# Kernel optimization log

Measured on AMD Instinct MI355X. Metric: run time of the kernel, lower is better.

## Reference

```python
import jax, jax.numpy as jnp
import numpy as np

B, S, D_VAL, D_AT = 4, 4096, 256, 256


def setup_inputs() -> dict:
    key = jax.random.key(0)
    k1, k2, k3, k4 = jax.random.split(key, 4)
    x = jax.random.normal(k1, (B, S, D_VAL), dtype=jnp.float32)
    # nn.Linear(d_in, d_out, bias=False) weight has shape [d_out, d_in]; y = x @ W.T
    Wq = jax.random.normal(k2, (D_AT, D_VAL), dtype=jnp.float32) * (1.0 / np.sqrt(D_VAL))
    Wk = jax.random.normal(k3, (D_AT, D_VAL), dtype=jnp.float32) * (1.0 / np.sqrt(D_VAL))
    Wv = jax.random.normal(k4, (D_VAL, D_VAL), dtype=jnp.float32) * (1.0 / np.sqrt(D_VAL))
    return {"x": x, "Wq": Wq, "Wk": Wk, "Wv": Wv}


def reference(x, Wq, Wk, Wv):
    # projections (Linear, no bias): x @ W.T
    q = jnp.einsum('bsd,ad->bsa', x, Wq)   # [B,S,d_at]
    k = jnp.einsum('bsd,ad->bsa', x, Wk)   # [B,S,d_at]
    v = jnp.einsum('bsd,ed->bse', x, Wv)   # [B,S,d_val]
    scale = 1.0 / jnp.sqrt(jnp.asarray(q.shape[-1], dtype=q.dtype))
    scores = jnp.einsum('bqa,bka->bqk', q, k) * scale  # [B,S,S]
    weights = jax.nn.softmax(scores, axis=-1)
    out = jnp.einsum('bqk,bke->bqe', weights, v)       # [B,S,d_val]
    return out
```

## Files before the change

kernel.cpp:

```cpp
#include <hip/hip_runtime.h>
#include <stdint.h>

#define B_ 4
#define S_ 4096
#define D_ 256
#define M_ (B_*S_)

typedef __attribute__((ext_vector_type(8))) short bf16x8;
typedef __attribute__((ext_vector_type(8))) unsigned short u16x8;
typedef __attribute__((ext_vector_type(4))) float f32x4;
typedef __attribute__((ext_vector_type(4))) unsigned short u16x4;

static __device__ __forceinline__ unsigned short f2bf(float f) {
  union { float f; unsigned u; } v; v.f = f;
  unsigned r = v.u + 0x7fffu + ((v.u >> 16) & 1u);
  return (unsigned short)(r >> 16);
}
static __device__ __forceinline__ float bf2f(unsigned short h) {
  union { unsigned u; float f; } v; v.u = ((unsigned)h) << 16;
  return v.f;
}

__global__ void cvt_kernel(const float* __restrict__ src, unsigned short* __restrict__ dst,
                           int n4) {
  int i = blockIdx.x * blockDim.x + threadIdx.x;
  int stride = gridDim.x * blockDim.x;
  for (; i < n4; i += stride) {
    float4 v = reinterpret_cast<const float4*>(src)[i];
    u16x4 o;
    o.x = f2bf(v.x); o.y = f2bf(v.y);
    o.z = f2bf(v.z); o.w = f2bf(v.w);
    reinterpret_cast<u16x4*>(dst)[i] = o;
  }
}

__global__ void cvt_w_kernel(const float* __restrict__ Wq, const float* __restrict__ Wk,
                             const float* __restrict__ Wv,
                             unsigned short* __restrict__ wqb, unsigned short* __restrict__ wkb,
                             unsigned short* __restrict__ wvb) {
  const int m = blockIdx.y;
  const float* src = (m == 0) ? Wq : (m == 1) ? Wk : Wv;
  unsigned short* dst = (m == 0) ? wqb : (m == 1) ? wkb : wvb;
  const float scale = (m == 0) ? 0.0625f * 1.44269504f : 1.0f;
  int i = blockIdx.x * 256 + threadIdx.x;
  int frag = i >> 6, lane = i & 63;
  int kc = frag >> 4, n = frag & 15;
  int lr = lane & 15, lh = lane >> 4;
  const float* sp = src + (size_t)(n * 16 + lr) * D_ + kc * 32 + lh * 8;
  float4 a = reinterpret_cast<const float4*>(sp)[0];
  float4 b = reinterpret_cast<const float4*>(sp)[1];
  u16x8 o;
  o[0] = f2bf(a.x * scale); o[1] = f2bf(a.y * scale);
  o[2] = f2bf(a.z * scale); o[3] = f2bf(a.w * scale);
  o[4] = f2bf(b.x * scale); o[5] = f2bf(b.y * scale);
  o[6] = f2bf(b.z * scale); o[7] = f2bf(b.w * scale);
  *reinterpret_cast<u16x8*>(dst + (size_t)frag * 512 + lane * 8) = o;
}

__global__ __launch_bounds__(256, 3) void proj_kernel(
    const unsigned short* __restrict__ xb,
    const unsigned short* __restrict__ wq,
    const unsigned short* __restrict__ wk,
    const unsigned short* __restrict__ wv,
    unsigned short* __restrict__ q_ws,
    unsigned short* __restrict__ k_ws,
    unsigned short* __restrict__ vt_ws) {
  const int mat = blockIdx.y;
  const unsigned short* wb = (mat == 0) ? wq : (mat == 1) ? wk : wv;
  const int tid = threadIdx.x;
  const int wave = tid >> 6, lane = tid & 63;
  const int lr = lane & 15, lh = lane >> 4;
  const int row0 = blockIdx.x * 64 + wave * 16;

  const f32x4 zero = {0.f, 0.f, 0.f, 0.f};

  bf16x8 af[8];
  {
    const unsigned short* xp = xb + (size_t)(row0 + lr) * D_ + lh * 8;
    #pragma unroll
    for (int kc = 0; kc < 8; kc++)
      af[kc] = *reinterpret_cast<const bf16x8*>(xp + kc * 32);
  }

  f32x4 acc[16];
  #pragma unroll
  for (int n = 0; n < 16; n++) acc[n] = zero;

  #pragma unroll
  for (int kc = 0; kc < 8; kc++) {
    #pragma unroll
    for (int n = 0; n < 16; n++) {
      bf16x8 wf = *reinterpret_cast<const bf16x8*>(wb + (size_t)(kc * 16 + n) * 512 + lane * 8);
      acc[n] = __builtin_amdgcn_mfma_f32_16x16x32_bf16(af[kc], wf, acc[n], 0, 0, 0);
    }
  }

  const int b  = row0 >> 12;
  const int s0 = row0 & 4095;
  const int t2 = s0 >> 5;
  const int w1 = wave & 1;

  if (mat == 0) {
    #pragma unroll
    for (int n = 0; n < 16; n++) {
      int col = n * 16 + lr;
      #pragma unroll
      for (int r = 0; r < 4; r++) {
        int row = row0 + lh * 4 + r;
        q_ws[(size_t)row * D_ + col] = f2bf(acc[n][r]);
      }
    }
  } else if (mat == 1) {
    char* tb = reinterpret_cast<char*>(k_ws) + ((size_t)(b * 128 + t2)) * 16384;
    #pragma unroll
    for (int n = 0; n < 16; n++) {
      int base = (w1 * 8 + (n >> 1)) * 1024 +
                 (((n & 1) << 1) | (lr >> 3)) * 256 +
                 lh * 64 + (lr & 7) * 2;
      #pragma unroll
      for (int r = 0; r < 4; r++)
        *reinterpret_cast<unsigned short*>(tb + base + r * 16) = f2bf(acc[n][r]);
    }
  } else {
    char* tb = reinterpret_cast<char*>(vt_ws) + ((size_t)(b * 128 + t2)) * 16384;
    #pragma unroll
    for (int n = 0; n < 16; n++) {
      u16x4 o;
      o.x = f2bf(acc[n][0]); o.y = f2bf(acc[n][1]);
      o.z = f2bf(acc[n][2]); o.w = f2bf(acc[n][3]);
      *reinterpret_cast<u16x4*>(tb + n * 1024 + lh * 256 + lr * 16 + w1 * 8) = o;
    }
  }
}

__global__ __launch_bounds__(256, 2) void attn_kernel(
    const unsigned short* __restrict__ q_ws,
    const unsigned short* __restrict__ k_ws,
    const unsigned short* __restrict__ vt_ws,
    unsigned short* __restrict__ po, float* __restrict__ pm, float* __restrict__ pl) {
  __shared__ char lds[2][32768];

  const int bid0 = blockIdx.x;
  const int xcd = bid0 & 7, idx = bid0 >> 3;
  const int b = xcd >> 1;
  const int h = (xcd & 1) * 2 + (idx >> 5);
  const int qt = idx & 31;
  const int tid = threadIdx.x;
  const int wave = tid >> 6, lane = tid & 63;
  const int lr = lane & 15, lh = lane >> 4;

  const int qrow0 = b * S_ + qt * 128 + wave * 32;

  bf16x8 qfA[8], qfB[8];
  {
    const unsigned short* qpA = q_ws + (size_t)(qrow0 + lr) * D_ + lh * 8;
    const unsigned short* qpB = qpA + 16 * D_;
    #pragma unroll
    for (int kc = 0; kc < 8; kc++) {
      qfA[kc] = *reinterpret_cast<const bf16x8*>(qpA + kc * 32);
      qfB[kc] = *reinterpret_cast<const bf16x8*>(qpB + kc * 32);
    }
  }

  f32x4 oaccA[16], oaccB[16];
  const f32x4 zero = {0.f, 0.f, 0.f, 0.f};
  #pragma unroll
  for (int n = 0; n < 16; n++) { oaccA[n] = zero; oaccB[n] = zero; }
  float mA = -1e30f, mB = -1e30f, lA = 0.f, lB = 0.f;

  const char* kgb = reinterpret_cast<const char*>(k_ws) + ((size_t)(b * 128 + h * 32)) * 16384;
  const char* vgb = reinterpret_cast<const char*>(vt_ws) + ((size_t)(b * 128 + h * 32)) * 16384;

  auto stage = [&](int t, int buf) {
    const char* kg = kgb + (size_t)t * 16384;
    const char* vg = vgb + (size_t)t * 16384;
    char* lk = lds[buf];
    char* lv = lds[buf] + 16384;
    #pragma unroll
    for (int i = 0; i < 4; i++) {
      __builtin_amdgcn_global_load_lds(
        (__attribute__((address_space(1))) void*)(void*)(kg + i * 4096 + tid * 16),
        (__attribute__((address_space(3))) void*)(lk + i * 4096 + tid * 16),
        16, 0, 0);
    }
    #pragma unroll
    for (int i = 0; i < 4; i++) {
      __builtin_amdgcn_global_load_lds(
        (__attribute__((address_space(1))) void*)(void*)(vg + i * 4096 + tid * 16),
        (__attribute__((address_space(3))) void*)(lv + i * 4096 + tid * 16),
        16, 0, 0);
    }
  };

  stage(0, 0);
  __syncthreads();

  for (int t = 0; t < 32; t++) {
    const int cur = t & 1;
    if (t + 1 < 32) stage(t + 1, cur ^ 1);

    const char* lk = lds[cur];
    const char* lv = lds[cur] + 16384;

    f32x4 sA0 = zero, sA1 = zero, sB0 = zero, sB1 = zero;
    __builtin_amdgcn_s_setprio(1);
    #pragma unroll
    for (int kc = 0; kc < 8; kc++) {
      bf16x8 kf0 = *reinterpret_cast<const bf16x8*>(lk + kc * 1024 + lane * 16);
      bf16x8 kf1 = *reinterpret_cast<const bf16x8*>(lk + (8 + kc) * 1024 + lane * 16);
      sA0 = __builtin_amdgcn_mfma_f32_16x16x32_bf16(kf0, qfA[kc], sA0, 0, 0, 0);
      sA1 = __builtin_amdgcn_mfma_f32_16x16x32_bf16(kf1, qfA[kc], sA1, 0, 0, 0);
      sB0 = __builtin_amdgcn_mfma_f32_16x16x32_bf16(kf0, qfB[kc], sB0, 0, 0, 0);
      sB1 = __builtin_amdgcn_mfma_f32_16x16x32_bf16(kf1, qfB[kc], sB1, 0, 0, 0);
    }
    __builtin_amdgcn_s_setprio(0);

    float pmaxA = fmaxf(fmaxf(fmaxf(sA0[0], sA0[1]), fmaxf(sA0[2], sA0[3])),
                        fmaxf(fmaxf(sA1[0], sA1[1]), fmaxf(sA1[2], sA1[3])));
    float pmaxB = fmaxf(fmaxf(fmaxf(sB0[0], sB0[1]), fmaxf(sB0[2], sB0[3])),
                        fmaxf(fmaxf(sB1[0], sB1[1]), fmaxf(sB1[2], sB1[3])));
    pmaxA = fmaxf(pmaxA, __shfl_xor(pmaxA, 16));
    pmaxA = fmaxf(pmaxA, __shfl_xor(pmaxA, 32));
    pmaxB = fmaxf(pmaxB, __shfl_xor(pmaxB, 16));
    pmaxB = fmaxf(pmaxB, __shfl_xor(pmaxB, 32));

    if (!__all((pmaxA - mA <= 8.f) & (pmaxB - mB <= 8.f))) {
      float miA = fmaxf(mA, pmaxA), miB = fmaxf(mB, pmaxB);
      float aA = exp2f(mA - miA), aB = exp2f(mB - miB);
      mA = miA; mB = miB; lA *= aA; lB *= aB;
      #pragma unroll
      for (int r = 0; r < 4; r++) {
        float avA = __shfl(aA, lh * 4 + r);
        float avB = __shfl(aB, lh * 4 + r);
        #pragma unroll
        for (int n = 0; n < 16; n++) { oaccA[n][r] *= avA; oaccB[n][r] *= avB; }
      }
    }

    bf16x8 paA, paB;
    float sumA = 0.f, sumB = 0.f;
    #pragma unroll
    for (int j = 0; j < 8; j++) {
      float vA = (j < 4) ? sA0[j & 3] : sA1[j & 3];
      float vB = (j < 4) ? sB0[j & 3] : sB1[j & 3];
      float pA = exp2f(vA - mA);
      float pB = exp2f(vB - mB);
      sumA += pA; sumB += pB;
      paA[j] = (short)f2bf(pA);
      paB[j] = (short)f2bf(pB);
    }
    sumA += __shfl_xor(sumA, 16); sumA += __shfl_xor(sumA, 32);
    sumB += __shfl_xor(sumB, 16); sumB += __shfl_xor(sumB, 32);
    lA += sumA; lB += sumB;

    __builtin_amdgcn_s_setprio(1);
    #pragma unroll
    for (int n = 0; n < 16; n++) {
      bf16x8 vf = *reinterpret_cast<const bf16x8*>(lv + n * 1024 + lane * 16);
      oaccA[n] = __builtin_amdgcn_mfma_f32_16x16x32_bf16(paA, vf, oaccA[n], 0, 0, 0);
      oaccB[n] = __builtin_amdgcn_mfma_f32_16x16x32_bf16(paB, vf, oaccB[n], 0, 0, 0);
    }
    __builtin_amdgcn_s_setprio(0);

    __syncthreads();
  }

  char* pwv = &lds[0][0] + wave * 16384;
  #pragma unroll
  for (int n = 0; n < 16; n++) {
    int colb = (n * 16 + lr) * 2;
    #pragma unroll
    for (int r = 0; r < 4; r++) {
      *reinterpret_cast<unsigned short*>(pwv + (lh * 4 + r) * 512 + colb) = f2bf(oaccA[n][r]);
      *reinterpret_cast<unsigned short*>(pwv + (16 + lh * 4 + r) * 512 + colb) = f2bf(oaccB[n][r]);
    }
  }
  __syncthreads();
  {
    unsigned short* pob = po + ((size_t)h * 16384 + qrow0) * D_;
    #pragma unroll
    for (int i = 0; i < 16; i++) {
      int off = i * 1024 + lane * 16;
      bf16x8 v = *reinterpret_cast<const bf16x8*>(pwv + off);
      int row = off >> 9, colb = off & 511;
      *reinterpret_cast<bf16x8*>(reinterpret_cast<char*>(pob) + row * 512 + colb) = v;
    }
  }
  if (lh == 0) { pm[(size_t)h * 16384 + qrow0 + lr] = mA; pl[(size_t)h * 16384 + qrow0 + lr] = lA; }
  if (lh == 1) { pm[(size_t)h * 16384 + qrow0 + 16 + lr] = mB; pl[(size_t)h * 16384 + qrow0 + 16 + lr] = lB; }
}

__global__ __launch_bounds__(256) void merge_kernel(
    const unsigned short* __restrict__ po, const float* __restrict__ pm,
    const float* __restrict__ pl, float* __restrict__ out) {
  int idx = blockIdx.x * 256 + threadIdx.x;
  int row = idx >> 5, c8 = idx & 31;
  float m0 = pm[row], m1 = pm[16384 + row], m2 = pm[32768 + row], m3 = pm[49152 + row];
  float l0 = pl[row], l1 = pl[16384 + row], l2 = pl[32768 + row], l3 = pl[49152 + row];
  float M = fmaxf(fmaxf(m0, m1), fmaxf(m2, m3));
  float a0 = exp2f(m0 - M), a1 = exp2f(m1 - M), a2 = exp2f(m2 - M), a3 = exp2f(m3 - M);
  float inv = 1.0f / (l0 * a0 + l1 * a1 + l2 * a2 + l3 * a3);
  float acc[8];
  #pragma unroll
  for (int j = 0; j < 8; j++) acc[j] = 0.f;
  const float aw[4] = {a0, a1, a2, a3};
  #pragma unroll
  for (int hh = 0; hh < 4; hh++) {
    u16x8 v = *reinterpret_cast<const u16x8*>(po + ((size_t)hh * 16384 + row) * D_ + c8 * 8);
    #pragma unroll
    for (int j = 0; j < 8; j++) acc[j] += aw[hh] * bf2f(v[j]);
  }
  float4 o0, o1;
  o0.x = acc[0] * inv; o0.y = acc[1] * inv; o0.z = acc[2] * inv; o0.w = acc[3] * inv;
  o1.x = acc[4] * inv; o1.y = acc[5] * inv; o1.z = acc[6] * inv; o1.w = acc[7] * inv;
  float4* op = reinterpret_cast<float4*>(out + (size_t)row * D_ + c8 * 8);
  op[0] = o0; op[1] = o1;
}

extern "C" void kernel_launch(void* const* d_in, const int* in_sizes, int n_in,
                              void* d_out, int out_size, void* d_ws, size_t ws_size,
                              hipStream_t stream) {
  const float* x  = (const float*)d_in[0];
  const float* Wq = (const float*)d_in[1];
  const float* Wk = (const float*)d_in[2];
  const float* Wv = (const float*)d_in[3];
  float* out = (float*)d_out;

  char* ws = (char*)d_ws;
  unsigned short* xb    = (unsigned short*)(ws);
  unsigned short* wqb   = (unsigned short*)(ws + 8388608);
  unsigned short* wkb   = (unsigned short*)(ws + 8519680);
  unsigned short* wvb   = (unsigned short*)(ws + 8650752);
  unsigned short* q_ws  = (unsigned short*)(ws + 8781824);
  unsigned short* k_ws  = (unsigned short*)(ws + 17170432);
  unsigned short* vt_ws = (unsigned short*)(ws + 25559040);
  unsigned short* po    = (unsigned short*)(ws + 33947648);
  float*          pm    = (float*)(ws + 67502080);
  float*          pl    = (float*)(ws + 67764224);

  cvt_kernel<<<1024, 256, 0, stream>>>(x, xb, M_ * D_ / 4);
  cvt_w_kernel<<<dim3(32, 3), 256, 0, stream>>>(Wq, Wk, Wv, wqb, wkb, wvb);
  proj_kernel<<<dim3(256, 3), 256, 0, stream>>>(xb, wqb, wkb, wvb, q_ws, k_ws, vt_ws);
  attn_kernel<<<512, 256, 0, stream>>>(q_ws, k_ws, vt_ws, po, pm, pl);
  merge_kernel<<<2048, 256, 0, stream>>>(po, pm, pl, out);
}
```

Baseline: 183.0 us.

## Fuse x conversion into projection and double query rows per attention wave

The standalone fp32-to-bf16 conversion kernel for x is removed, and the projection kernel now reads fp32 x and converts it in registers. The attention kernel now gives each wave 64 query rows (four 16-row groups) instead of 32, so every K/V tile staged in LDS is reused across twice as many rows. The grid is halved to 256 blocks with occupancy 1. The intent is to cut the extra pass over x and the K/V load traffic per query row, at the cost of much higher register pressure and fewer resident waves for hiding latency.

```diff
diff --git a/kernel.cpp b/kernel.cpp
--- a/kernel.cpp
+++ b/kernel.cpp
@@ -19,19 +19,6 @@
 static __device__ __forceinline__ float bf2f(unsigned short h) {
   union { unsigned u; float f; } v; v.u = ((unsigned)h) << 16;
   return v.f;
-}
-
-__global__ void cvt_kernel(const float* __restrict__ src, unsigned short* __restrict__ dst,
-                           int n4) {
-  int i = blockIdx.x * blockDim.x + threadIdx.x;
-  int stride = gridDim.x * blockDim.x;
-  for (; i < n4; i += stride) {
-    float4 v = reinterpret_cast<const float4*>(src)[i];
-    u16x4 o;
-    o.x = f2bf(v.x); o.y = f2bf(v.y);
-    o.z = f2bf(v.z); o.w = f2bf(v.w);
-    reinterpret_cast<u16x4*>(dst)[i] = o;
-  }
 }
 
 __global__ void cvt_w_kernel(const float* __restrict__ Wq, const float* __restrict__ Wk,
@@ -58,7 +45,7 @@
 }
 
 __global__ __launch_bounds__(256, 3) void proj_kernel(
-    const unsigned short* __restrict__ xb,
+    const float* __restrict__ x,
     const unsigned short* __restrict__ wq,
     const unsigned short* __restrict__ wk,
     const unsigned short* __restrict__ wv,
@@ -76,10 +63,18 @@
 
   bf16x8 af[8];
   {
-    const unsigned short* xp = xb + (size_t)(row0 + lr) * D_ + lh * 8;
-    #pragma unroll
-    for (int kc = 0; kc < 8; kc++)
-      af[kc] = *reinterpret_cast<const bf16x8*>(xp + kc * 32);
+    const float* xp = x + (size_t)(row0 + lr) * D_ + lh * 8;
+    #pragma unroll
+    for (int kc = 0; kc < 8; kc++) {
+      float4 a = *reinterpret_cast<const float4*>(xp + kc * 32);
+      float4 c = *reinterpret_cast<const float4*>(xp + kc * 32 + 4);
+      bf16x8 f;
+      f[0] = (short)f2bf(a.x); f[1] = (short)f2bf(a.y);
+      f[2] = (short)f2bf(a.z); f[3] = (short)f2bf(a.w);
+      f[4] = (short)f2bf(c.x); f[5] = (short)f2bf(c.y);
+      f[6] = (short)f2bf(c.z); f[7] = (short)f2bf(c.w);
+      af[kc] = f;
+    }
   }
 
   f32x4 acc[16];
@@ -133,7 +128,7 @@
   }
 }
 
-__global__ __launch_bounds__(256, 2) void attn_kernel(
+__global__ __launch_bounds__(256, 1) void attn_kernel(
     const unsigned short* __restrict__ q_ws,
     const unsigned short* __restrict__ k_ws,
     const unsigned short* __restrict__ vt_ws,
@@ -143,30 +138,32 @@
   const int bid0 = blockIdx.x;
   const int xcd = bid0 & 7, idx = bid0 >> 3;
   const int b = xcd >> 1;
-  const int h = (xcd & 1) * 2 + (idx >> 5);
-  const int qt = idx & 31;
+  const int h = (xcd & 1) * 2 + (idx >> 4);
+  const int qt = idx & 15;
   const int tid = threadIdx.x;
   const int wave = tid >> 6, lane = tid & 63;
   const int lr = lane & 15, lh = lane >> 4;
 
-  const int qrow0 = b * S_ + qt * 128 + wave * 32;
-
-  bf16x8 qfA[8], qfB[8];
-  {
-    const unsigned short* qpA = q_ws + (size_t)(qrow0 + lr) * D_ + lh * 8;
-    const unsigned short* qpB = qpA + 16 * D_;
-    #pragma unroll
-    for (int kc = 0; kc < 8; kc++) {
-      qfA[kc] = *reinterpret_cast<const bf16x8*>(qpA + kc * 32);
-      qfB[kc] = *reinterpret_cast<const bf16x8*>(qpB + kc * 32);
-    }
-  }
-
-  f32x4 oaccA[16], oaccB[16];
+  const int qrow0 = b * S_ + qt * 256 + wave * 64;
+
+  bf16x8 qf[4][8];
+  #pragma unroll
+  for (int G = 0; G < 4; G++) {
+    const unsigned short* qp = q_ws + (size_t)(qrow0 + G * 16 + lr) * D_ + lh * 8;
+    #pragma unroll
+    for (int kc = 0; kc < 8; kc++)
+      qf[G][kc] = *reinterpret_cast<const bf16x8*>(qp + kc * 32);
+  }
+
+  f32x4 oacc[4][16];
   const f32x4 zero = {0.f, 0.f, 0.f, 0.f};
   #pragma unroll
-  for (int n = 0; n < 16; n++) { oaccA[n] = zero; oaccB[n] = zero; }
-  float mA = -1e30f, mB = -1e30f, lA = 0.f, lB = 0.f;
+  for (int G = 0; G < 4; G++)
+    #pragma unroll
+    for (int n = 0; n < 16; n++) oacc[G][n] = zero;
+  float m[4], l[4];
+  #pragma unroll
+  for (int G = 0; G < 4; G++) { m[G] = -1e30f; l[G] = 0.f; }
 
   const char* kgb = reinterpret_cast<const char*>(k_ws) + ((size_t)(b * 128 + h * 32)) * 16384;
   const char* vgb = reinterpret_cast<const char*>(vt_ws) + ((size_t)(b * 128 + h * 32)) * 16384;
@@ -202,82 +199,95 @@
     const char* lk = lds[cur];
     const char* lv = lds[cur] + 16384;
 
-    f32x4 sA0 = zero, sA1 = zero, sB0 = zero, sB1 = zero;
+    f32x4 s[4][2];
+    #pragma unroll
+    for (int G = 0; G < 4; G++) { s[G][0] = zero; s[G][1] = zero; }
     __builtin_amdgcn_s_setprio(1);
     #pragma unroll
     for (int kc = 0; kc < 8; kc++) {
       bf16x8 kf0 = *reinterpret_cast<const bf16x8*>(lk + kc * 1024 + lane * 16);
       bf16x8 kf1 = *reinterpret_cast<const bf16x8*>(lk + (8 + kc) * 1024 + lane * 16);
-      sA0 = __builtin_amdgcn_mfma_f32_16x16x32_bf16(kf0, qfA[kc], sA0, 0, 0, 0);
-      sA1 = __builtin_amdgcn_mfma_f32_16x16x32_bf16(kf1, qfA[kc], sA1, 0, 0, 0);
-      sB0 = __builtin_amdgcn_mfma_f32_16x16x32_bf16(kf0, qfB[kc], sB0, 0, 0, 0);
-      sB1 = __builtin_amdgcn_mfma_f32_16x16x32_bf16(kf1, qfB[kc], sB1, 0, 0, 0);
+      #pragma unroll
+      for (int G = 0; G < 4; G++) {
+        s[G][0] = __builtin_amdgcn_mfma_f32_16x16x32_bf16(kf0, qf[G][kc], s[G][0], 0, 0, 0);
+        s[G][1] = __builtin_amdgcn_mfma_f32_16x16x32_bf16(kf1, qf[G][kc], s[G][1], 0, 0, 0);
+      }
     }
     __builtin_amdgcn_s_setprio(0);
 
-    float pmaxA = fmaxf(fmaxf(fmaxf(sA0[0], sA0[1]), fmaxf(sA0[2], sA0[3])),
-                        fmaxf(fmaxf(sA1[0], sA1[1]), fmaxf(sA1[2], sA1[3])));
-    float pmaxB = fmaxf(fmaxf(fmaxf(sB0[0], sB0[1]), fmaxf(sB0[2], sB0[3])),
-                        fmaxf(fmaxf(sB1[0], sB1[1]), fmaxf(sB1[2], sB1[3])));
-    pmaxA = fmaxf(pmaxA, __shfl_xor(pmaxA, 16));
-    pmaxA = fmaxf(pmaxA, __shfl_xor(pmaxA, 32));
-    pmaxB = fmaxf(pmaxB, __shfl_xor(pmaxB, 16));
-    pmaxB = fmaxf(pmaxB, __shfl_xor(pmaxB, 32));
-
-    if (!__all((pmaxA - mA <= 8.f) & (pmaxB - mB <= 8.f))) {
-      float miA = fmaxf(mA, pmaxA), miB = fmaxf(mB, pmaxB);
-      float aA = exp2f(mA - miA), aB = exp2f(mB - miB);
-      mA = miA; mB = miB; lA *= aA; lB *= aB;
-      #pragma unroll
-      for (int r = 0; r < 4; r++) {
-        float avA = __shfl(aA, lh * 4 + r);
-        float avB = __shfl(aB, lh * 4 + r);
+    float pmax[4];
+    #pragma unroll
+    for (int G = 0; G < 4; G++) {
+      float mx = fmaxf(fmaxf(fmaxf(s[G][0][0], s[G][0][1]), fmaxf(s[G][0][2], s[G][0][3])),
+                       fmaxf(fmaxf(s[G][1][0], s[G][1][1]), fmaxf(s[G][1][2], s[G][1][3])));
+      mx = fmaxf(mx, __shfl_xor(mx, 16));
+      mx = fmaxf(mx, __shfl_xor(mx, 32));
+      pmax[G] = mx;
+    }
+
+    int ok = (pmax[0] - m[0] <= 8.f) & (pmax[1] - m[1] <= 8.f) &
+             (pmax[2] - m[2] <= 8.f) & (pmax[3] - m[3] <= 8.f);
+    if (!__all(ok)) {
+      #pragma unroll
+      for (int G = 0; G < 4; G++) {
+        float mi = fmaxf(m[G], pmax[G]);
+        float a = exp2f(m[G] - mi);
+        m[G] = mi; l[G] *= a;
         #pragma unroll
-        for (int n = 0; n < 16; n++) { oaccA[n][r] *= avA; oaccB[n][r] *= avB; }
-      }
-    }
-
-    bf16x8 paA, paB;
-    float sumA = 0.f, sumB = 0.f;
-    #pragma unroll
-    for (int j = 0; j < 8; j++) {
-      float vA = (j < 4) ? sA0[j & 3] : sA1[j & 3];
-      float vB = (j < 4) ? sB0[j & 3] : sB1[j & 3];
-      float pA = exp2f(vA - mA);
-      float pB = exp2f(vB - mB);
-      sumA += pA; sumB += pB;
-      paA[j] = (short)f2bf(pA);
-      paB[j] = (short)f2bf(pB);
-    }
-    sumA += __shfl_xor(sumA, 16); sumA += __shfl_xor(sumA, 32);
-    sumB += __shfl_xor(sumB, 16); sumB += __shfl_xor(sumB, 32);
-    lA += sumA; lB += sumB;
+        for (int r = 0; r < 4; r++) {
+          float av = __shfl(a, lh * 4 + r);
+          #pragma unroll
+          for (int n = 0; n < 16; n++) oacc[G][n][r] *= av;
+        }
+      }
+    }
+
+    bf16x8 pa[4];
+    #pragma unroll
+    for (int G = 0; G < 4; G++) {
+      float sum = 0.f;
+      #pragma unroll
+      for (int j = 0; j < 8; j++) {
+        float v = (j < 4) ? s[G][0][j & 3] : s[G][1][j & 3];
+        float p = exp2f(v - m[G]);
+        sum += p;
+        pa[G][j] = (short)f2bf(p);
+      }
+      sum += __shfl_xor(sum, 16);
+      sum += __shfl_xor(sum, 32);
+      l[G] += sum;
+    }
 
     __builtin_amdgcn_s_setprio(1);
     #pragma unroll
     for (int n = 0; n < 16; n++) {
       bf16x8 vf = *reinterpret_cast<const bf16x8*>(lv + n * 1024 + lane * 16);
-      oaccA[n] = __builtin_amdgcn_mfma_f32_16x16x32_bf16(paA, vf, oaccA[n], 0, 0, 0);
-      oaccB[n] = __builtin_amdgcn_mfma_f32_16x16x32_bf16(paB, vf, oaccB[n], 0, 0, 0);
+      #pragma unroll
+      for (int G = 0; G < 4; G++)
+        oacc[G][n] = __builtin_amdgcn_mfma_f32_16x16x32_bf16(pa[G], vf, oacc[G][n], 0, 0, 0);
     }
     __builtin_amdgcn_s_setprio(0);
 
     __syncthreads();
   }
 
+  __syncthreads();
   char* pwv = &lds[0][0] + wave * 16384;
   #pragma unroll
-  for (int n = 0; n < 16; n++) {
-    int colb = (n * 16 + lr) * 2;
-    #pragma unroll
-    for (int r = 0; r < 4; r++) {
-      *reinterpret_cast<unsigned short*>(pwv + (lh * 4 + r) * 512 + colb) = f2bf(oaccA[n][r]);
-      *reinterpret_cast<unsigned short*>(pwv + (16 + lh * 4 + r) * 512 + colb) = f2bf(oaccB[n][r]);
-    }
-  }
-  __syncthreads();
-  {
-    unsigned short* pob = po + ((size_t)h * 16384 + qrow0) * D_;
+  for (int p = 0; p < 2; p++) {
+    #pragma unroll
+    for (int g2 = 0; g2 < 2; g2++) {
+      int G = p * 2 + g2;
+      #pragma unroll
+      for (int n = 0; n < 16; n++) {
+        int colb = (n * 16 + lr) * 2;
+        #pragma unroll
+        for (int r = 0; r < 4; r++)
+          *reinterpret_cast<unsigned short*>(pwv + (g2 * 16 + lh * 4 + r) * 512 + colb) =
+              f2bf(oacc[G][n][r]);
+      }
+    }
+    unsigned short* pob = po + ((size_t)h * 16384 + qrow0 + p * 32) * D_;
     #pragma unroll
     for (int i = 0; i < 16; i++) {
       int off = i * 1024 + lane * 16;
@@ -286,8 +296,13 @@
       *reinterpret_cast<bf16x8*>(reinterpret_cast<char*>(pob) + row * 512 + colb) = v;
     }
   }
-  if (lh == 0) { pm[(size_t)h * 16384 + qrow0 + lr] = mA; pl[(size_t)h * 16384 + qrow0 + lr] = lA; }
-  if (lh == 1) { pm[(size_t)h * 16384 + qrow0 + 16 + lr] = mB; pl[(size_t)h * 16384 + qrow0 + 16 + lr] = lB; }
+  #pragma unroll
+  for (int G = 0; G < 4; G++) {
+    if (lh == G) {
+      pm[(size_t)h * 16384 + qrow0 + G * 16 + lr] = m[G];
+      pl[(size_t)h * 16384 + qrow0 + G * 16 + lr] = l[G];
+    }
+  }
 }
 
 __global__ __launch_bounds__(256) void merge_kernel(
@@ -327,7 +342,6 @@
   float* out = (float*)d_out;
 
   char* ws = (char*)d_ws;
-  unsigned short* xb    = (unsigned short*)(ws);
   unsigned short* wqb   = (unsigned short*)(ws + 8388608);
   unsigned short* wkb   = (unsigned short*)(ws + 8519680);
   unsigned short* wvb   = (unsigned short*)(ws + 8650752);
@@ -338,9 +352,8 @@
   float*          pm    = (float*)(ws + 67502080);
   float*          pl    = (float*)(ws + 67764224);
 
-  cvt_kernel<<<1024, 256, 0, stream>>>(x, xb, M_ * D_ / 4);
   cvt_w_kernel<<<dim3(32, 3), 256, 0, stream>>>(Wq, Wk, Wv, wqb, wkb, wvb);
-  proj_kernel<<<dim3(256, 3), 256, 0, stream>>>(xb, wqb, wkb, wvb, q_ws, k_ws, vt_ws);
-  attn_kernel<<<512, 256, 0, stream>>>(q_ws, k_ws, vt_ws, po, pm, pl);
+  proj_kernel<<<dim3(256, 3), 256, 0, stream>>>(x, wqb, wkb, wvb, q_ws, k_ws, vt_ws);
+  attn_kernel<<<256, 256, 0, stream>>>(q_ws, k_ws, vt_ws, po, pm, pl);
   merge_kernel<<<2048, 256, 0, stream>>>(po, pm, pl, out);
 }
```

New measurement: 641.6 us. 3.51x slower.
